# Performance work log

Hardware: AMD Instinct MI355X
Metric: run time of the kernel (lower is better)

Reference implementation:

```python
import jax, jax.numpy as jnp
import numpy as np

D_MODEL = 1024
N_HEADS = 16
D_K = D_MODEL // N_HEADS


def setup_inputs() -> dict:
    key = jax.random.key(0)
    ks = jax.random.split(key, 9)
    s = 1.0 / np.sqrt(D_MODEL)
    x = jax.random.normal(ks[0], (2, 2048, D_MODEL), dtype=jnp.float32)
    Wq = jax.random.uniform(ks[1], (D_MODEL, D_MODEL), jnp.float32, -s, s)
    bq = jax.random.uniform(ks[2], (D_MODEL,), jnp.float32, -s, s)
    Wk = jax.random.uniform(ks[3], (D_MODEL, D_MODEL), jnp.float32, -s, s)
    bk = jax.random.uniform(ks[4], (D_MODEL,), jnp.float32, -s, s)
    Wv = jax.random.uniform(ks[5], (D_MODEL, D_MODEL), jnp.float32, -s, s)
    bv = jax.random.uniform(ks[6], (D_MODEL,), jnp.float32, -s, s)
    Wo = jax.random.uniform(ks[7], (D_MODEL, D_MODEL), jnp.float32, -s, s)
    bo = jax.random.uniform(ks[8], (D_MODEL,), jnp.float32, -s, s)
    return {"x": x, "Wq": Wq, "bq": bq, "Wk": Wk, "bk": bk,
            "Wv": Wv, "bv": bv, "Wo": Wo, "bo": bo}


def reference(x, Wq, bq, Wk, bk, Wv, bv, Wo, bo):
    B, S, _ = x.shape
    # torch Linear: y = x @ W.T + b
    def proj(W, b):
        h = x @ W.T + b                       # [B,S,D]
        return h.reshape(B, S, N_HEADS, D_K).transpose(0, 2, 1, 3)  # [B,H,S,dk]
    Q, K, V = proj(Wq, bq), proj(Wk, bk), proj(Wv, bv)
    scale = 1.0 / np.sqrt(D_K).astype(np.float32)
    scores = jnp.einsum('bhqd,bhkd->bhqk', Q, K) * scale  # [B,H,S,S]
    causal = jnp.tril(jnp.ones((S, S), dtype=bool))
    scores = jnp.where(causal, scores, -jnp.inf)
    attn = jax.nn.softmax(scores, axis=-1)
    ctx = jnp.einsum('bhqk,bhkd->bhqd', attn, V)          # [B,H,S,dk]
    ctx = ctx.transpose(0, 2, 1, 3).reshape(B, S, D_MODEL)
    return ctx @ Wo.T + bo
```

## Files before the change

### kernel.cpp

```cpp
#include <hip/hip_runtime.h>
#include <stdint.h>

#define D_MODEL 1024
#define NHEADS  16
#define DKH     64
#define BATCH   2
#define SEQ     2048
#define NTOK    (BATCH*SEQ)

typedef unsigned short u16;
typedef __attribute__((ext_vector_type(8))) short short8;
typedef __attribute__((ext_vector_type(4))) float f32x4;
typedef __attribute__((ext_vector_type(16))) float f32x16;
typedef __attribute__((ext_vector_type(2))) unsigned int u32x2;
typedef __attribute__((address_space(1))) unsigned int as1_u32;
typedef __attribute__((address_space(3))) unsigned int as3_u32;

__device__ __forceinline__ u16 f2bf(float f) {
  unsigned int i = __float_as_uint(f);
  i += 0x7FFF + ((i >> 16) & 1);
  return (u16)(i >> 16);
}
__device__ __forceinline__ f32x4 mfma_bf16(short8 a, short8 b, f32x4 c) {
  return __builtin_amdgcn_mfma_f32_16x16x32_bf16(a, b, c, 0, 0, 0);
}
__device__ __forceinline__ f32x16 mfma32(short8 a, short8 b, f32x16 c) {
  return __builtin_amdgcn_mfma_f32_32x32x16_bf16(a, b, c, 0, 0, 0);
}
__device__ __forceinline__ void gload_lds16(const u16* g, u16* l) {
  __builtin_amdgcn_global_load_lds((as1_u32*)g, (as3_u32*)l, 16, 0, 0);
}
__device__ __forceinline__ short8 ld_frag(const u16* p) {
  short8 v; __builtin_memcpy(&v, __builtin_assume_aligned(p, 16), 16); return v;
}
__device__ __forceinline__ void ld16(uint32_t* dst4, const void* src) {
  __builtin_memcpy(dst4, __builtin_assume_aligned(src, 16), 16);
}
__device__ __forceinline__ void st16(u16* dst, const uint32_t* src4) {
  __builtin_memcpy(__builtin_assume_aligned(dst, 16), src4, 16);
}
__device__ __forceinline__ uint32_t pk_bf16_trunc(float hi, float lo) {
  return __builtin_amdgcn_perm(__float_as_uint(hi), __float_as_uint(lo), 0x07060302u);
}

#define QSCALE 0.18033688011112042f
#define M0LOG2 4.32808512266689f

__global__ __launch_bounds__(256)
void convert_kernel(const float* __restrict__ x,  const float* __restrict__ wq,
                    const float* __restrict__ wk, const float* __restrict__ wv,
                    const float* __restrict__ wo,
                    u16* __restrict__ xb,  u16* __restrict__ wqb,
                    u16* __restrict__ wkb, u16* __restrict__ wvb,
                    u16* __restrict__ wob)
{
  const int q = blockIdx.x * 256 + threadIdx.x;
  const float* src; u16* dst; int local;
  if (q < 1048576) { src = x; dst = xb; local = q; }
  else {
    const int t = q - 1048576, r = t >> 18;
    local = t & 262143;
    src = (r == 0) ? wq : (r == 1) ? wk : (r == 2) ? wv : wo;
    dst = (r == 0) ? wqb : (r == 1) ? wkb : (r == 2) ? wvb : wob;
  }
  float f[4];
  __builtin_memcpy(f, src + (size_t)local * 4, 16);
  uint32_t o[2];
  o[0] = ((uint32_t)f2bf(f[1]) << 16) | f2bf(f[0]);
  o[1] = ((uint32_t)f2bf(f[3]) << 16) | f2bf(f[2]);
  __builtin_memcpy(dst + (size_t)local * 4, o, 8);
}

__device__ __forceinline__ void gemm_core_bf16(
    const u16* __restrict__ A, const u16* __restrict__ Bt,
    int m0, int n0, u16* As, u16* Bs, f32x4 (&acc)[4][4])
{
  const int tid  = threadIdx.x;
  const int wave = tid >> 6, lane = tid & 63;
  const int quad = lane >> 4, l15 = lane & 15;
  const int wm = wave & 1, wn = wave >> 1;
  const int srow = lane >> 2;
  const int scol = (lane & 3) << 3;

#pragma unroll
  for (int i = 0; i < 4; i++)
#pragma unroll
    for (int j = 0; j < 4; j++) acc[i][j] = (f32x4){0.f, 0.f, 0.f, 0.f};

  for (int k0 = 0; k0 < D_MODEL; k0 += 32) {
    __syncthreads();
#pragma unroll
    for (int is = 0; is < 2; is++) {
      const int rbase = (is * 4 + wave) * 16;
      gload_lds16(A  + (size_t)(m0 + rbase + srow) * D_MODEL + k0 + scol, As + rbase * 32);
      gload_lds16(Bt + (size_t)(n0 + rbase + srow) * D_MODEL + k0 + scol, Bs + rbase * 32);
    }
    __syncthreads();

    short8 aF[4], bF[4];
#pragma unroll
    for (int i = 0; i < 4; i++)
      aF[i] = ld_frag(As + (wm * 64 + i * 16 + l15) * 32 + quad * 8);
#pragma unroll
    for (int j = 0; j < 4; j++)
      bF[j] = ld_frag(Bs + (wn * 64 + j * 16 + l15) * 32 + quad * 8);
#pragma unroll
    for (int i = 0; i < 4; i++)
#pragma unroll
      for (int j = 0; j < 4; j++)
        acc[i][j] = mfma_bf16(aF[i], bF[j], acc[i][j]);
  }
}

__global__ __launch_bounds__(256)
void qkv_proj_kernel(const u16* __restrict__ xb,
                     const u16* __restrict__ Wqb, const u16* __restrict__ Wkb,
                     const u16* __restrict__ Wvb,
                     const float* __restrict__ bq, const float* __restrict__ bk,
                     const float* __restrict__ bv,
                     u16* __restrict__ qplane, u16* __restrict__ ws)
{
  __shared__ __align__(16) u16 As[128 * 32];
  __shared__ __align__(16) u16 Bs[128 * 32];

  const int m0  = blockIdx.x * 128;
  const int by  = blockIdx.y;
  const int mat = by >> 3;
  const int n0  = (by & 7) * 128;
  const u16* W      = (mat == 0) ? Wqb : (mat == 1) ? Wkb : Wvb;
  const float* bias = (mat == 0) ? bq : (mat == 1) ? bk : bv;
  u16* out = (mat == 0) ? qplane : ws + (size_t)(mat - 1) * ((size_t)NTOK * D_MODEL);
  const float scale = (mat == 0) ? QSCALE : 1.0f;

  f32x4 acc[4][4];
  gemm_core_bf16(xb, W, m0, n0, As, Bs, acc);

  const int tid = threadIdx.x, wave = tid >> 6, lane = tid & 63;
  const int quad = lane >> 4, l15 = lane & 15;
  const int wm = wave & 1, wn = wave >> 1;
#pragma unroll
  for (int j = 0; j < 4; j++) {
    const int gcol = n0 + wn * 64 + j * 16 + l15;
    const float bias_v = bias[gcol];
    const int h = gcol >> 6, dj = gcol & 63;
#pragma unroll
    for (int i = 0; i < 4; i++) {
#pragma unroll
      for (int r = 0; r < 4; r++) {
        const int grow = m0 + wm * 64 + i * 16 + quad * 4 + r;
        const int b = grow >> 11, s = grow & (SEQ - 1);
        const float v = (acc[i][j][r] + bias_v) * scale;
        out[(((size_t)(b * NHEADS + h)) * SEQ + s) * DKH + dj] = f2bf(v);
      }
    }
  }
}


__device__ __forceinline__ void storeVt(u16* Vt, const uint32_t* va,
                                        const uint32_t* vb, int r2, int cV) {
#pragma unroll
  for (int j = 0; j < 8; j++) {
    const int d = cV + j;
    const uint32_t w = __builtin_amdgcn_perm(vb[j >> 1], va[j >> 1],
                         (j & 1) ? 0x07060302u : 0x05040100u);
    __builtin_memcpy(Vt + d * 64 + (r2 ^ ((d & 7) << 3)), &w, 4);
  }
}

__device__ __forceinline__ void soft_pack(const f32x16& s, const int khBase,
                                          const bool diag, const int qloc,
                                          const int h4, float& l_acc,
                                          short8& fA, short8& fB) {
  float pv[16];
#pragma unroll
  for (int rr = 0; rr < 16; rr++) {
    float v = exp2f(s[rr]);
    if (diag) {
      const int kloc = khBase + (rr & 3) + 8 * (rr >> 2) + h4;
      if (kloc > qloc) v = 0.f;
    }
    pv[rr] = v;
  }
  const float t0 = (pv[0] + pv[1]) + (pv[2] + pv[3]);
  const float t1 = (pv[4] + pv[5]) + (pv[6] + pv[7]);
  const float t2 = (pv[8] + pv[9]) + (pv[10] + pv[11]);
  const float t3 = (pv[12] + pv[13]) + (pv[14] + pv[15]);
  l_acc += (t0 + t1) + (t2 + t3);
  uint32_t w[2][4];
#pragma unroll
  for (int ks = 0; ks < 2; ks++) {
    const uint32_t x0 = pk_bf16_trunc(pv[8 * ks + 1], pv[8 * ks + 0]);
    const uint32_t x1 = pk_bf16_trunc(pv[8 * ks + 3], pv[8 * ks + 2]);
    const uint32_t y0 = pk_bf16_trunc(pv[8 * ks + 5], pv[8 * ks + 4]);
    const uint32_t y1 = pk_bf16_trunc(pv[8 * ks + 7], pv[8 * ks + 6]);
    const u32x2 r0 = __builtin_amdgcn_permlane32_swap(x0, y0, false, false);
    const u32x2 r1 = __builtin_amdgcn_permlane32_swap(x1, y1, false, false);
    w[ks][0] = r0[0]; w[ks][1] = r1[0]; w[ks][2] = r0[1]; w[ks][3] = r1[1];
  }
  __builtin_memcpy(&fA, &w[0][0], 16);
  __builtin_memcpy(&fB, &w[1][0], 16);
}

__device__ __forceinline__ void osum_write(float* OS, const f32x16& o0,
                                           const f32x16& o1, int qb, int l31) {
#pragma unroll
  for (int rr = 0; rr < 16; rr++) {
    const int q = qb + (rr & 3) + 8 * (rr >> 2);
    OS[q * 64 + l31]      = o0[rr];
    OS[q * 64 + 32 + l31] = o1[rr];
  }
}
__device__ __forceinline__ void osum_add(const float* OS, f32x16& o0,
                                         f32x16& o1, int qb, int l31) {
#pragma unroll
  for (int rr = 0; rr < 16; rr++) {
    const int q = qb + (rr & 3) + 8 * (rr >> 2);
    o0[rr] += OS[q * 64 + l31];
    o1[rr] += OS[q * 64 + 32 + l31];
  }
}

__global__ __launch_bounds__(512, 4)
void attn_kernel(const u16* __restrict__ Qp, const u16* __restrict__ Kp,
                 const u16* __restrict__ Vp, u16* __restrict__ ctx)
{
  __shared__ __align__(16) u16 Ks[2][2][64 * 64];
  __shared__ __align__(16) u16 Vts[2][2][64 * 64];

  const int xp = blockIdx.x;
  const int bh = blockIdx.y;
  const u16* Q = Qp + (size_t)bh * SEQ * DKH;
  const u16* K = Kp + (size_t)bh * SEQ * DKH;
  const u16* V = Vp + (size_t)bh * SEQ * DKH;

  const int tid  = threadIdx.x;
  const int w    = tid >> 6;
  const int lane = tid & 63;
  const int l31  = lane & 31, h = lane >> 5, h8 = h * 8;
  const int g    = w >> 2;
  const int wq   = (w >> 1) & 1;
  const int kh   = w & 1;
  const int pg   = g * 2 + kh;
  const int ktid = tid & 255;
  const int rK = ktid >> 2, cK = (ktid & 3) * 16;
  const int krx = (rK & 7) << 3;
  const int r2 = (ktid & 31) * 2, cV = ((ktid >> 5) & 7) * 8;
  const int b = bh >> 4, hd = bh & 15;
  const int qloc = wq * 32 + l31;
  const int qb   = wq * 32 + h * 4;
  const int xr   = (l31 & 7) << 3;
  const int khB  = kh * 32;

  float* Osum0 = (float*)&Ks[0][0][0];
  float* Osum1 = (float*)&Ks[1][0][0];
  float* Ls    = (float*)&Vts[0][0][0];

#pragma unroll
  for (int p = 0; p < 2; p++) {
    const int qt = p ? xp : 31 - xp;
    const int q0 = qt * 64;
    const int maxR = (qt >> 1) + 1;

    const short8 qf0 = ld_frag(Q + (size_t)(q0 + qloc) * DKH + 0  + h8);
    const short8 qf1 = ld_frag(Q + (size_t)(q0 + qloc) * DKH + 16 + h8);
    const short8 qf2 = ld_frag(Q + (size_t)(q0 + qloc) * DKH + 32 + h8);
    const short8 qf3 = ld_frag(Q + (size_t)(q0 + qloc) * DKH + 48 + h8);

    uint32_t ka[4], kb[4], va[4], vb[4];
    const bool act0 = (g <= qt);
    if (act0) {
      const int kn = g * 64;
      ld16(ka, K + (size_t)(kn + rK) * DKH + cK);
      ld16(kb, K + (size_t)(kn + rK) * DKH + cK + 8);
      ld16(va, V + (size_t)(kn + r2) * DKH + cV);
      ld16(vb, V + (size_t)(kn + r2 + 1) * DKH + cV);
    }
    __syncthreads();
    if (act0) {
      st16(&Ks[g][0][0] + rK * 64 + (cK ^ krx), ka);
      st16(&Ks[g][0][0] + rK * 64 + ((cK + 8) ^ krx), kb);
      storeVt(&Vts[g][0][0], va, vb, r2, cV);
    }
    float l_acc = 0.f;
    f32x16 oacc0, oacc1;
#pragma unroll
    for (int rr = 0; rr < 16; rr++) { oacc0[rr] = 0.f; oacc1[rr] = 0.f; }
    __syncthreads();

    for (int r = 0; r < maxR; r++) {
      const int kt = 2 * r + g;
      const int buf = r & 1;
      const bool act = (kt <= qt);
      const bool pre = (kt + 2 <= qt);
      const u16* ksb = &Ks[g][buf][0];
      const u16* vtb = &Vts[g][buf][0];
      if (pre) {
        const int kn = (kt + 2) * 64;
        ld16(ka, K + (size_t)(kn + rK) * DKH + cK);
        ld16(kb, K + (size_t)(kn + rK) * DKH + cK + 8);
        ld16(va, V + (size_t)(kn + r2) * DKH + cV);
        ld16(vb, V + (size_t)(kn + r2 + 1) * DKH + cV);
      }
      if (act) {
        f32x16 s;
#pragma unroll
        for (int rr = 0; rr < 16; rr++) s[rr] = -M0LOG2;
        const u16* kbase = ksb + (size_t)(khB + l31) * 64;
        s = mfma32(ld_frag(kbase + ((0  + h8) ^ xr)), qf0, s);
        s = mfma32(ld_frag(kbase + ((16 + h8) ^ xr)), qf1, s);
        s = mfma32(ld_frag(kbase + ((32 + h8) ^ xr)), qf2, s);
        s = mfma32(ld_frag(kbase + ((48 + h8) ^ xr)), qf3, s);
        short8 pa0, pa1;
        soft_pack(s, khB, kt == qt, qloc, h * 4, l_acc, pa0, pa1);
        const u16* v0 = vtb + (size_t)l31 * 64;
        const u16* v1 = vtb + (size_t)(32 + l31) * 64;
        oacc0 = mfma32(pa0, ld_frag(v0 + ((khB + 0  + h8) ^ xr)), oacc0);
        oacc1 = mfma32(pa0, ld_frag(v1 + ((khB + 0  + h8) ^ xr)), oacc1);
        oacc0 = mfma32(pa1, ld_frag(v0 + ((khB + 16 + h8) ^ xr)), oacc0);
        oacc1 = mfma32(pa1, ld_frag(v1 + ((khB + 16 + h8) ^ xr)), oacc1);
      }
      if (pre) {
        u16* ksN = &Ks[g][buf ^ 1][0];
        st16(ksN + rK * 64 + (cK ^ krx), ka);
        st16(ksN + rK * 64 + ((cK + 8) ^ krx), kb);
        storeVt(&Vts[g][buf ^ 1][0], va, vb, r2, cV);
      }
      __syncthreads();
    }

    l_acc += __shfl_xor(l_acc, 32);
    if (lane < 32) Ls[pg * 64 + wq * 32 + l31] = l_acc;
    if (pg == 1) osum_write(Osum0, oacc0, oacc1, qb, l31);
    if (pg == 3) osum_write(Osum1, oacc0, oacc1, qb, l31);
    __syncthreads();
    if (pg == 0) osum_add(Osum0, oacc0, oacc1, qb, l31);
    if (pg == 2) osum_add(Osum1, oacc0, oacc1, qb, l31);
    if (w == 1) {
      const float sum = Ls[lane] + Ls[64 + lane] + Ls[128 + lane] + Ls[192 + lane];
      Ls[lane] = 1.f / sum;
    }
    __syncthreads();
    if (pg == 2) osum_write(Osum0, oacc0, oacc1, qb, l31);
    __syncthreads();
    if (pg == 0) {
#pragma unroll
      for (int rr = 0; rr < 16; rr++) {
        const int q = qb + (rr & 3) + 8 * (rr >> 2);
        const float linv = Ls[q];
        u16* dst = ctx + ((size_t)(b * SEQ + q0 + q)) * D_MODEL + hd * DKH;
        dst[l31]      = f2bf((oacc0[rr] + Osum0[q * 64 + l31]) * linv);
        dst[32 + l31] = f2bf((oacc1[rr] + Osum0[q * 64 + 32 + l31]) * linv);
      }
    }
  }
}

__global__ __launch_bounds__(256)
void oproj_kernel(const u16* __restrict__ ctx, const u16* __restrict__ Wob,
                  const float* __restrict__ bo, float* __restrict__ out)
{
  __shared__ __align__(16) u16 As[128 * 32];
  __shared__ __align__(16) u16 Bs[128 * 32];
  const int m0 = blockIdx.x * 128, n0 = blockIdx.y * 128;

  f32x4 acc[4][4];
  gemm_core_bf16(ctx, Wob, m0, n0, As, Bs, acc);

  const int tid = threadIdx.x, wave = tid >> 6, lane = tid & 63;
  const int quad = lane >> 4, l15 = lane & 15;
  const int wm = wave & 1, wn = wave >> 1;
#pragma unroll
  for (int j = 0; j < 4; j++) {
    const int gcol = n0 + wn * 64 + j * 16 + l15;
    const float bias_v = bo[gcol];
#pragma unroll
    for (int i = 0; i < 4; i++) {
#pragma unroll
      for (int r = 0; r < 4; r++) {
        const int grow = m0 + wm * 64 + i * 16 + quad * 4 + r;
        out[(size_t)grow * D_MODEL + gcol] = acc[i][j][r] + bias_v;
      }
    }
  }
}

extern "C" void kernel_launch(void* const* d_in, const int* in_sizes, int n_in,
                              void* d_out, int out_size, void* d_ws, size_t ws_size,
                              hipStream_t stream) {
  const float* x  = (const float*)d_in[0];
  const float* Wq = (const float*)d_in[1];
  const float* bq = (const float*)d_in[2];
  const float* Wk = (const float*)d_in[3];
  const float* bk = (const float*)d_in[4];
  const float* Wv = (const float*)d_in[5];
  const float* bv = (const float*)d_in[6];
  const float* Wo = (const float*)d_in[7];
  const float* bo = (const float*)d_in[8];
  u16*   ws   = (u16*)d_ws;
  u16*   o16  = (u16*)d_out;
  float* out  = (float*)d_out;

  const size_t plane = (size_t)NTOK * D_MODEL;
  u16* Kp  = ws;
  u16* Vp  = ws + plane;
  u16* xb  = ws + 2 * plane;
  u16* ctx = ws + 2 * plane;
  u16* Wob = ws + 3 * plane;
  u16* Qp  = o16;
  u16* Wqb = o16 + 4 * 1048576;
  u16* Wkb = o16 + 5 * 1048576;
  u16* Wvb = o16 + 6 * 1048576;

  convert_kernel<<<dim3(8192), dim3(256), 0, stream>>>(x, Wq, Wk, Wv, Wo,
                                                       xb, Wqb, Wkb, Wvb, Wob);
  qkv_proj_kernel<<<dim3(32, 24), dim3(256), 0, stream>>>(xb, Wqb, Wkb, Wvb,
                                                          bq, bk, bv, Qp, ws);
  attn_kernel<<<dim3(16, 32), dim3(512), 0, stream>>>(Qp, Kp, Vp, ctx);
  oproj_kernel<<<dim3(32, 8), dim3(256), 0, stream>>>(ctx, Wob, bo, out);
}
```

Before: 222.8 us.

## Pre-swizzle K/V tiles in projection epilogue and stage via direct global-to-LDS loads

The QKV projection epilogue now writes K and V in per-64-row tile layouts that already carry the LDS XOR swizzle, with V stored transposed. The attention kernel can then copy each tile into shared memory with contiguous global_load_lds DMA instead of loading into registers, permuting, and storing. This removes the VGPR staging and the V transpose work from the attention inner loop. In exchange the projection epilogue does scattered transposed stores, and the LDS writes are asynchronous, so correctness depends on the existing barriers covering completion of the DMA loads.

```diff
diff --git a/kernel.cpp b/kernel.cpp
--- a/kernel.cpp
+++ b/kernel.cpp
@@ -32,12 +32,6 @@
 }
 __device__ __forceinline__ short8 ld_frag(const u16* p) {
   short8 v; __builtin_memcpy(&v, __builtin_assume_aligned(p, 16), 16); return v;
-}
-__device__ __forceinline__ void ld16(uint32_t* dst4, const void* src) {
-  __builtin_memcpy(dst4, __builtin_assume_aligned(src, 16), 16);
-}
-__device__ __forceinline__ void st16(u16* dst, const uint32_t* src4) {
-  __builtin_memcpy(__builtin_assume_aligned(dst, 16), src4, 16);
 }
 __device__ __forceinline__ uint32_t pk_bf16_trunc(float hi, float lo) {
   return __builtin_amdgcn_perm(__float_as_uint(hi), __float_as_uint(lo), 0x07060302u);
@@ -118,7 +112,8 @@
                      const u16* __restrict__ Wvb,
                      const float* __restrict__ bq, const float* __restrict__ bk,
                      const float* __restrict__ bv,
-                     u16* __restrict__ qplane, u16* __restrict__ ws)
+                     u16* __restrict__ qplane, u16* __restrict__ kplane,
+                     u16* __restrict__ vplane)
 {
   __shared__ __align__(16) u16 As[128 * 32];
   __shared__ __align__(16) u16 Bs[128 * 32];
@@ -129,8 +124,6 @@
   const int n0  = (by & 7) * 128;
   const u16* W      = (mat == 0) ? Wqb : (mat == 1) ? Wkb : Wvb;
   const float* bias = (mat == 0) ? bq : (mat == 1) ? bk : bv;
-  u16* out = (mat == 0) ? qplane : ws + (size_t)(mat - 1) * ((size_t)NTOK * D_MODEL);
-  const float scale = (mat == 0) ? QSCALE : 1.0f;
 
   f32x4 acc[4][4];
   gemm_core_bf16(xb, W, m0, n0, As, Bs, acc);
@@ -138,35 +131,64 @@
   const int tid = threadIdx.x, wave = tid >> 6, lane = tid & 63;
   const int quad = lane >> 4, l15 = lane & 15;
   const int wm = wave & 1, wn = wave >> 1;
-#pragma unroll
-  for (int j = 0; j < 4; j++) {
-    const int gcol = n0 + wn * 64 + j * 16 + l15;
-    const float bias_v = bias[gcol];
-    const int h = gcol >> 6, dj = gcol & 63;
-#pragma unroll
-    for (int i = 0; i < 4; i++) {
-#pragma unroll
-      for (int r = 0; r < 4; r++) {
-        const int grow = m0 + wm * 64 + i * 16 + quad * 4 + r;
-        const int b = grow >> 11, s = grow & (SEQ - 1);
-        const float v = (acc[i][j][r] + bias_v) * scale;
-        out[(((size_t)(b * NHEADS + h)) * SEQ + s) * DKH + dj] = f2bf(v);
-      }
-    }
-  }
-}
-
-
-__device__ __forceinline__ void storeVt(u16* Vt, const uint32_t* va,
-                                        const uint32_t* vb, int r2, int cV) {
-#pragma unroll
-  for (int j = 0; j < 8; j++) {
-    const int d = cV + j;
-    const uint32_t w = __builtin_amdgcn_perm(vb[j >> 1], va[j >> 1],
-                         (j & 1) ? 0x07060302u : 0x05040100u);
-    __builtin_memcpy(Vt + d * 64 + (r2 ^ ((d & 7) << 3)), &w, 4);
-  }
-}
+
+  if (mat == 0) {
+#pragma unroll
+    for (int j = 0; j < 4; j++) {
+      const int gcol = n0 + wn * 64 + j * 16 + l15;
+      const float bias_v = bias[gcol];
+      const int h = gcol >> 6, dj = gcol & 63;
+#pragma unroll
+      for (int i = 0; i < 4; i++) {
+#pragma unroll
+        for (int r = 0; r < 4; r++) {
+          const int grow = m0 + wm * 64 + i * 16 + quad * 4 + r;
+          const int b = grow >> 11, s = grow & (SEQ - 1);
+          const float v = (acc[i][j][r] + bias_v) * QSCALE;
+          qplane[(((size_t)(b * NHEADS + h)) * SEQ + s) * DKH + dj] = f2bf(v);
+        }
+      }
+    }
+  } else if (mat == 1) {
+#pragma unroll
+    for (int j = 0; j < 4; j++) {
+      const int gcol = n0 + wn * 64 + j * 16 + l15;
+      const float bias_v = bias[gcol];
+      const int h = gcol >> 6, dj = gcol & 63;
+#pragma unroll
+      for (int i = 0; i < 4; i++) {
+#pragma unroll
+        for (int r = 0; r < 4; r++) {
+          const int grow = m0 + wm * 64 + i * 16 + quad * 4 + r;
+          const int b = grow >> 11, s = grow & (SEQ - 1);
+          const int kt = s >> 6, rr = s & 63;
+          kplane[(((size_t)(b * NHEADS + h)) * 32 + kt) * 4096
+                 + rr * 64 + (dj ^ ((rr & 7) << 3))] = f2bf(acc[i][j][r] + bias_v);
+        }
+      }
+    }
+  } else {
+#pragma unroll
+    for (int j = 0; j < 4; j++) {
+      const int gcol = n0 + wn * 64 + j * 16 + l15;
+      const float bias_v = bias[gcol];
+      const int h = gcol >> 6, dj = gcol & 63;
+      const int vswz = (dj & 7) << 3;
+#pragma unroll
+      for (int i = 0; i < 4; i++) {
+#pragma unroll
+        for (int r = 0; r < 4; r++) {
+          const int grow = m0 + wm * 64 + i * 16 + quad * 4 + r;
+          const int b = grow >> 11, s = grow & (SEQ - 1);
+          const int kt = s >> 6, kk = s & 63;
+          vplane[(((size_t)(b * NHEADS + h)) * 32 + kt) * 4096
+                 + dj * 64 + (kk ^ vswz)] = f2bf(acc[i][j][r] + bias_v);
+        }
+      }
+    }
+  }
+}
+
 
 __device__ __forceinline__ void soft_pack(const f32x16& s, const int khBase,
                                           const bool diag, const int qloc,
@@ -221,31 +243,38 @@
   }
 }
 
+__device__ __forceinline__ void stage_tile(const u16* gsrc, u16* ldst,
+                                           int w4, int lane8) {
+#pragma unroll
+  for (int i = 0; i < 2; i++) {
+    const int chunk = (w4 * 2 + i) * 512;
+    gload_lds16(gsrc + chunk + lane8, ldst + chunk);
+  }
+}
+
 __global__ __launch_bounds__(512, 4)
 void attn_kernel(const u16* __restrict__ Qp, const u16* __restrict__ Kp,
                  const u16* __restrict__ Vp, u16* __restrict__ ctx)
 {
-  __shared__ __align__(16) u16 Ks[2][2][64 * 64];
-  __shared__ __align__(16) u16 Vts[2][2][64 * 64];
+  __shared__ __align__(16) u16 Ks[2][2][4096];
+  __shared__ __align__(16) u16 Vts[2][2][4096];
 
   const int xp = blockIdx.x;
   const int bh = blockIdx.y;
-  const u16* Q = Qp + (size_t)bh * SEQ * DKH;
-  const u16* K = Kp + (size_t)bh * SEQ * DKH;
-  const u16* V = Vp + (size_t)bh * SEQ * DKH;
+  const u16* Q  = Qp + (size_t)bh * SEQ * DKH;
+  const u16* Kt = Kp + (size_t)bh * SEQ * DKH;
+  const u16* Vt = Vp + (size_t)bh * SEQ * DKH;
 
   const int tid  = threadIdx.x;
   const int w    = tid >> 6;
   const int lane = tid & 63;
+  const int lane8 = lane * 8;
   const int l31  = lane & 31, h = lane >> 5, h8 = h * 8;
   const int g    = w >> 2;
+  const int w4   = w & 3;
   const int wq   = (w >> 1) & 1;
   const int kh   = w & 1;
   const int pg   = g * 2 + kh;
-  const int ktid = tid & 255;
-  const int rK = ktid >> 2, cK = (ktid & 3) * 16;
-  const int krx = (rK & 7) << 3;
-  const int r2 = (ktid & 31) * 2, cV = ((ktid >> 5) & 7) * 8;
   const int b = bh >> 4, hd = bh & 15;
   const int qloc = wq * 32 + l31;
   const int qb   = wq * 32 + h * 4;
@@ -262,25 +291,17 @@
     const int q0 = qt * 64;
     const int maxR = (qt >> 1) + 1;
 
-    const short8 qf0 = ld_frag(Q + (size_t)(q0 + qloc) * DKH + 0  + h8);
-    const short8 qf1 = ld_frag(Q + (size_t)(q0 + qloc) * DKH + 16 + h8);
-    const short8 qf2 = ld_frag(Q + (size_t)(q0 + qloc) * DKH + 32 + h8);
-    const short8 qf3 = ld_frag(Q + (size_t)(q0 + qloc) * DKH + 48 + h8);
-
-    uint32_t ka[4], kb[4], va[4], vb[4];
+    const u16* qrow = Q + (size_t)(q0 + qloc) * DKH + h8;
+    const short8 qf0 = ld_frag(qrow + 0);
+    const short8 qf1 = ld_frag(qrow + 16);
+    const short8 qf2 = ld_frag(qrow + 32);
+    const short8 qf3 = ld_frag(qrow + 48);
+
+    __syncthreads();
     const bool act0 = (g <= qt);
     if (act0) {
-      const int kn = g * 64;
-      ld16(ka, K + (size_t)(kn + rK) * DKH + cK);
-      ld16(kb, K + (size_t)(kn + rK) * DKH + cK + 8);
-      ld16(va, V + (size_t)(kn + r2) * DKH + cV);
-      ld16(vb, V + (size_t)(kn + r2 + 1) * DKH + cV);
-    }
-    __syncthreads();
-    if (act0) {
-      st16(&Ks[g][0][0] + rK * 64 + (cK ^ krx), ka);
-      st16(&Ks[g][0][0] + rK * 64 + ((cK + 8) ^ krx), kb);
-      storeVt(&Vts[g][0][0], va, vb, r2, cV);
+      stage_tile(Kt + (size_t)g * 4096, &Ks[g][0][0],  w4, lane8);
+      stage_tile(Vt + (size_t)g * 4096, &Vts[g][0][0], w4, lane8);
     }
     float l_acc = 0.f;
     f32x16 oacc0, oacc1;
@@ -292,39 +313,27 @@
       const int kt = 2 * r + g;
       const int buf = r & 1;
       const bool act = (kt <= qt);
-      const bool pre = (kt + 2 <= qt);
-      const u16* ksb = &Ks[g][buf][0];
-      const u16* vtb = &Vts[g][buf][0];
-      if (pre) {
-        const int kn = (kt + 2) * 64;
-        ld16(ka, K + (size_t)(kn + rK) * DKH + cK);
-        ld16(kb, K + (size_t)(kn + rK) * DKH + cK + 8);
-        ld16(va, V + (size_t)(kn + r2) * DKH + cV);
-        ld16(vb, V + (size_t)(kn + r2 + 1) * DKH + cV);
+      if (kt + 2 <= qt) {
+        stage_tile(Kt + (size_t)(kt + 2) * 4096, &Ks[g][buf ^ 1][0],  w4, lane8);
+        stage_tile(Vt + (size_t)(kt + 2) * 4096, &Vts[g][buf ^ 1][0], w4, lane8);
       }
       if (act) {
         f32x16 s;
 #pragma unroll
         for (int rr = 0; rr < 16; rr++) s[rr] = -M0LOG2;
-        const u16* kbase = ksb + (size_t)(khB + l31) * 64;
+        const u16* kbase = &Ks[g][buf][0] + (size_t)(khB + l31) * 64;
         s = mfma32(ld_frag(kbase + ((0  + h8) ^ xr)), qf0, s);
         s = mfma32(ld_frag(kbase + ((16 + h8) ^ xr)), qf1, s);
         s = mfma32(ld_frag(kbase + ((32 + h8) ^ xr)), qf2, s);
         s = mfma32(ld_frag(kbase + ((48 + h8) ^ xr)), qf3, s);
         short8 pa0, pa1;
         soft_pack(s, khB, kt == qt, qloc, h * 4, l_acc, pa0, pa1);
-        const u16* v0 = vtb + (size_t)l31 * 64;
-        const u16* v1 = vtb + (size_t)(32 + l31) * 64;
+        const u16* v0 = &Vts[g][buf][0] + (size_t)l31 * 64;
+        const u16* v1 = &Vts[g][buf][0] + (size_t)(32 + l31) * 64;
         oacc0 = mfma32(pa0, ld_frag(v0 + ((khB + 0  + h8) ^ xr)), oacc0);
         oacc1 = mfma32(pa0, ld_frag(v1 + ((khB + 0  + h8) ^ xr)), oacc1);
         oacc0 = mfma32(pa1, ld_frag(v0 + ((khB + 16 + h8) ^ xr)), oacc0);
         oacc1 = mfma32(pa1, ld_frag(v1 + ((khB + 16 + h8) ^ xr)), oacc1);
-      }
-      if (pre) {
-        u16* ksN = &Ks[g][buf ^ 1][0];
-        st16(ksN + rK * 64 + (cK ^ krx), ka);
-        st16(ksN + rK * 64 + ((cK + 8) ^ krx), kb);
-        storeVt(&Vts[g][buf ^ 1][0], va, vb, r2, cV);
       }
       __syncthreads();
     }
@@ -415,7 +424,7 @@
   convert_kernel<<<dim3(8192), dim3(256), 0, stream>>>(x, Wq, Wk, Wv, Wo,
                                                        xb, Wqb, Wkb, Wvb, Wob);
   qkv_proj_kernel<<<dim3(32, 24), dim3(256), 0, stream>>>(xb, Wqb, Wkb, Wvb,
-                                                          bq, bk, bv, Qp, ws);
+                                                          bq, bk, bv, Qp, Kp, Vp);
   attn_kernel<<<dim3(16, 32), dim3(512), 0, stream>>>(Qp, Kp, Vp, ctx);
   oproj_kernel<<<dim3(32, 8), dim3(256), 0, stream>>>(ctx, Wob, bo, out);
 }
```

Result: faster. 207.0 us (-7.1%).
